# Kernel tuning notes

Measured on AMD Instinct MI355X. Metric: run time of the kernel, lower is better.

The kernel has to match this reference:

```python
import jax, jax.numpy as jnp
import numpy as np

N1 = 384
N2 = 384
E = 3072
NUM_LABELS = 32
GCN_SIZES = [128, 64, 32]
BIG = 99999.0


def gcn_conv(x, edge_index, w, b, n):
    # PyG GCNConv: add self-loops, symmetric deg^-1/2 normalization, x @ W then scatter-sum, + bias
    src, dst = edge_index[0], edge_index[1]
    loops = jnp.arange(n, dtype=src.dtype)
    src = jnp.concatenate([src, loops])
    dst = jnp.concatenate([dst, loops])
    deg = jax.ops.segment_sum(jnp.ones(src.shape[0], x.dtype), dst, num_segments=n)
    dinv = jnp.where(deg > 0, 1.0 / jnp.sqrt(deg), 0.0)
    norm = dinv[src] * dinv[dst]
    h = x @ w  # [n, out]
    return jax.ops.segment_sum(norm[:, None] * h[src], dst, num_segments=n) + b


def conv_pass(x, edge_index, ws, bs, n):
    feats = []
    for i in range(len(ws)):
        x = gcn_conv(x, edge_index, ws[i], bs[i], n)
        feats.append(x)
        if i < len(ws) - 1:
            x = jax.nn.relu(x)  # dropout inactive (eval mode)
    return feats


def build_cost_matrices(f1s, f2s, dels, inss, n1, n2):
    ins_const = BIG * (1.0 - jnp.eye(n1, dtype=jnp.float32))
    del_const = BIG * (1.0 - jnp.eye(n2, dtype=jnp.float32))
    mats = []
    for f1, f2, dp, ip in zip(f1s, f2s, dels, inss):
        main = -(f1 @ f2.T)                          # [n1, n2]
        del_sim = jnp.diag(-(f1 @ dp)) + ins_const   # [n1, n1]
        ins_sim = jnp.diag(-(f2 @ ip)) + del_const   # [n2, n2]
        dummy = jnp.zeros((n2, n1), jnp.float32)
        mats.append(jnp.block([[main, del_sim], [ins_sim, dummy]]))  # [n1+n2, n1+n2]
    return mats


def solve_lap(C):
    """Exact Jonker-Volgenant shortest-augmenting-path LAP (minimization),
    equivalent to lapjv / scipy linear_sum_assignment. Returns col4row."""
    C = np.asarray(C, dtype=np.float64)
    n = C.shape[0]
    u = np.zeros(n)
    v = np.zeros(n)
    row4col = np.full(n, -1, dtype=np.int64)
    col4row = np.full(n, -1, dtype=np.int64)
    for cur_row in range(n):
        shortest = np.full(n, np.inf)
        path = np.full(n, -1, dtype=np.int64)
        SR = np.zeros(n, dtype=bool)
        SC = np.zeros(n, dtype=bool)
        remaining = np.arange(n)
        num_rem = n
        min_val = 0.0
        i = cur_row
        sink = -1
        while sink == -1:
            SR[i] = True
            r = remaining[:num_rem]
            d = min_val + C[i, r] - u[i] - v[r]
            upd = d < shortest[r]
            ru = r[upd]
            shortest[ru] = d[upd]
            path[ru] = i
            k = int(np.argmin(shortest[r]))
            j = int(r[k])
            min_val = float(shortest[j])
            SC[j] = True
            num_rem -= 1
            remaining[k] = remaining[num_rem]
            if row4col[j] == -1:
                sink = j
            else:
                i = int(row4col[j])
        u[cur_row] += min_val
        other = SR.copy()
        other[cur_row] = False
        rows = np.nonzero(other)[0]
        if rows.size:
            u[rows] += min_val - shortest[col4row[rows]]
        cols = np.nonzero(SC)[0]
        v[cols] -= min_val - shortest[cols]
        j = sink
        while True:
            i = int(path[j])
            row4col[j] = i
            col4row[i], j = j, int(col4row[i])
            if i == cur_row:
                break
    return col4row


def setup_inputs() -> dict:
    key = jax.random.key(0)
    ks = jax.random.split(key, 24)
    inp = {}
    inp["edge_index_1"] = jax.random.randint(ks[0], (2, E), 0, N1, dtype=jnp.int32)
    inp["edge_index_2"] = jax.random.randint(ks[1], (2, E), 0, N2, dtype=jnp.int32)
    inp["features_1"] = jax.random.normal(ks[2], (N1, NUM_LABELS), jnp.float32)
    inp["features_2"] = jax.random.normal(ks[3], (N2, NUM_LABELS), jnp.float32)
    inp["n1"] = N1
    inp["n2"] = N2
    inp["avg_v"] = jnp.full((1,), (N1 + N2) / 2.0, jnp.float32)
    sizes = [NUM_LABELS] + GCN_SIZES
    for li in range(3):
        fan_in = sizes[li]
        inp[f"w{li+1}"] = jax.random.normal(ks[4 + 2 * li], (sizes[li], sizes[li + 1]), jnp.float32) / np.sqrt(fan_in)
        inp[f"b{li+1}"] = 0.01 * jax.random.normal(ks[5 + 2 * li], (sizes[li + 1],), jnp.float32)
        inp[f"del{li+1}"] = 0.1 * jax.random.normal(ks[10 + li], (GCN_SIZES[li],), jnp.float32)
        inp[f"ins{li+1}"] = 0.1 * jax.random.normal(ks[13 + li], (GCN_SIZES[li],), jnp.float32)
    inp["score_w"] = jax.random.normal(ks[16], (1, 3), jnp.float32) * 0.5
    inp["score_b"] = jax.random.normal(ks[17], (1,), jnp.float32) * 0.1
    return inp


def reference(edge_index_1, edge_index_2, features_1, features_2, n1, n2, avg_v,
              w1, b1, w2, b2, w3, b3, del1, del2, del3, ins1, ins2, ins3,
              score_w, score_b):
    ws, bs = (w1, w2, w3), (b1, b2, b3)
    f1s = conv_pass(features_1, edge_index_1, ws, bs, n1)
    f2s = conv_pass(features_2, edge_index_2, ws, bs, n2)
    mats = build_cost_matrices(f1s, f2s, (del1, del2, del3), (ins1, ins2, ins3), n1, n2)
    n = n1 + n2
    rows = jnp.arange(n)
    losses = []
    for S in mats:
        col = solve_lap(np.asarray(jax.device_get(S)))  # host LAP on detached costs
        losses.append(jnp.sum(S[rows, jnp.asarray(col, dtype=jnp.int32)]) / n)
    matching_cost = 2.0 * jnp.stack(losses) / (n1 + n2)  # [3]
    logits = score_w @ matching_cost + score_b           # [1]
    score = jax.nn.sigmoid(logits)
    pre_ged = -jnp.log(score) * avg_v                    # target_mode == 'exp'
    return score, pre_ged, matching_cost
```

## Files before the change

kernel.cpp:

```cpp
#include <hip/hip_runtime.h>
#include <math.h>


namespace {
constexpr int kN   = 384;
constexpr int kNN  = 768;
constexpr int kE   = 3072;
constexpr float kInf = 1e30f;
}

__device__ __forceinline__ float wave_min_bcast(float xv) {
    float v = xv;
    #define MSTAGE(ctrl) { int t = __builtin_amdgcn_update_dpp(__float_as_int(v), __float_as_int(v), ctrl, 0xF, 0xF, false); v = fminf(v, __int_as_float(t)); }
    MSTAGE(0x111); MSTAGE(0x112); MSTAGE(0x114); MSTAGE(0x118); MSTAGE(0x142); MSTAGE(0x143);
    #undef MSTAGE
    return __int_as_float(__builtin_amdgcn_readlane(__float_as_int(v), 63));
}

__device__ __forceinline__ float wave_sum_bcast(float x) {
    #define SSTAGE(ctrl) { int t = __builtin_amdgcn_update_dpp(0, __float_as_int(x), ctrl, 0xF, 0xF, false); x += __int_as_float(t); }
    SSTAGE(0x111); SSTAGE(0x112); SSTAGE(0x114); SSTAGE(0x118); SSTAGE(0x142); SSTAGE(0x143);
    #undef SSTAGE
    return __int_as_float(__builtin_amdgcn_readlane(__float_as_int(x), 63));
}

__device__ __forceinline__ void wave_min2_bcast(float m1, float m2, float& w1, float& w2) {
    const int INFB = __float_as_int(kInf);
    #define M2STAGE(ctrl) { \
        int t1 = __builtin_amdgcn_update_dpp(INFB, __float_as_int(m1), ctrl, 0xF, 0xF, false); \
        int t2 = __builtin_amdgcn_update_dpp(INFB, __float_as_int(m2), ctrl, 0xF, 0xF, false); \
        float o1 = __int_as_float(t1); float o2 = __int_as_float(t2); \
        float n2 = fminf(fmaxf(m1, o1), fminf(m2, o2)); \
        m1 = fminf(m1, o1); m2 = n2; }
    M2STAGE(0x111); M2STAGE(0x112); M2STAGE(0x114); M2STAGE(0x118); M2STAGE(0x142); M2STAGE(0x143);
    #undef M2STAGE
    w1 = __int_as_float(__builtin_amdgcn_readlane(__float_as_int(m1), 63));
    w2 = __int_as_float(__builtin_amdgcn_readlane(__float_as_int(m2), 63));
}


__global__ void init_deg(float* deg1, float* deg2) {
    int v = blockIdx.x * blockDim.x + threadIdx.x;
    if (v < kN) { deg1[v] = 1.0f; deg2[v] = 1.0f; }
}

__global__ void scatter_deg(const int* ei1, const int* ei2, float* deg1, float* deg2) {
    int e = blockIdx.x * blockDim.x + threadIdx.x;
    if (e < kE) {
        atomicAdd(&deg1[ei1[kE + e]], 1.0f);
    } else if (e < 2 * kE) {
        atomicAdd(&deg2[ei2[kE + (e - kE)]], 1.0f);
    }
}

__global__ void deg_to_dinv(float* deg1, float* deg2) {
    int v = blockIdx.x * blockDim.x + threadIdx.x;
    if (v < kN) { deg1[v] = rsqrtf(deg1[v]); deg2[v] = rsqrtf(deg2[v]); }
}


__global__ void gemm_act(const float* __restrict__ x, const float* __restrict__ w,
                         float* __restrict__ h, int FIN, int FOUT, int relu) {
    int idx = blockIdx.x * blockDim.x + threadIdx.x;
    if (idx >= kN * FOUT) return;
    int row = idx / FOUT;
    int oc  = idx - row * FOUT;
    float acc = 0.0f;
    for (int k = 0; k < FIN; ++k) {
        float xv = x[row * FIN + k];
        if (relu) xv = fmaxf(xv, 0.0f);
        acc += xv * w[k * FOUT + oc];
    }
    h[idx] = acc;
}

__global__ void agg_init(const float* __restrict__ h, const float* __restrict__ dinv,
                         const float* __restrict__ b, float* __restrict__ out, int F) {
    int idx = blockIdx.x * blockDim.x + threadIdx.x;
    if (idx >= kN * F) return;
    int v = idx / F;
    int f = idx - v * F;
    float dv = dinv[v];
    out[idx] = b[f] + dv * dv * h[idx];
}

__global__ void agg_edges(const int* __restrict__ ei, const float* __restrict__ h,
                          const float* __restrict__ dinv, float* __restrict__ out, int F) {
    int idx = blockIdx.x * blockDim.x + threadIdx.x;
    if (idx >= kE * F) return;
    int e = idx / F;
    int f = idx - e * F;
    int s = ei[e];
    int d = ei[kE + e];
    atomicAdd(&out[d * F + f], dinv[s] * dinv[d] * h[s * F + f]);
}


__global__ void node_dots(const float* __restrict__ f, const float* __restrict__ p,
                          float* __restrict__ out, int F) {
    int i = blockIdx.x * blockDim.x + threadIdx.x;
    if (i >= kN) return;
    float acc = 0.0f;
    for (int k = 0; k < F; ++k) acc += f[i * F + k] * p[k];
    out[i] = -acc;
}


__global__ void build_cost_red(const float* __restrict__ f1, const float* __restrict__ f2,
                               const float* __restrict__ D, const float* __restrict__ I,
                               float* __restrict__ C, float* __restrict__ CT, int have_ct,
                               unsigned* __restrict__ vbits, int F) {
    int j = blockIdx.x * blockDim.x + threadIdx.x;
    int i = blockIdx.y;
    if (j >= kN) return;
    float acc = 0.0f;
    for (int k = 0; k < F; ++k) acc += f1[i * F + k] * f2[j * F + k];
    float val = (-acc) - D[i] - I[j];
    float c = fminf(0.0f, val);
    C[i * kN + j] = c;
    if (have_ct) CT[(size_t)j * kN + i] = c;
    atomicMax(&vbits[j], __float_as_uint(c));
}


__global__ __launch_bounds__(64) void vb2v_scale(const unsigned* __restrict__ vbits,
                                                 float* __restrict__ v_sk,
                                                 float* __restrict__ s) {
    int m = blockIdx.x, lane = threadIdx.x;
    float a = 0.0f;
    for (int r = 0; r < 6; ++r) {
        int j = lane + 64 * r;
        float vv = __uint_as_float(vbits[m * kN + j]);
        v_sk[m * kN + j] = vv;
        a += fabsf(vv);
    }
    float tot = wave_sum_bcast(a);
    if (lane == 0) s[m] = fmaxf(tot / (float)kN, 1e-6f);
}

__global__ __launch_bounds__(64) void sk_row(const float* __restrict__ Call,
                                             const float* __restrict__ v_sk,
                                             float* __restrict__ u_sk,
                                             float tau, const float* __restrict__ s) {
    int i = blockIdx.x, m = blockIdx.y, lane = threadIdx.x;
    float t = tau * s[m];
    const float* R = Call + (size_t)m * kN * kN + (size_t)i * kN;
    float hh[6];
    float mn = kInf;
    #pragma unroll
    for (int r = 0; r < 6; ++r) {
        int j = lane + 64 * r;
        hh[r] = R[j] - v_sk[m * kN + j];
        mn = fminf(mn, hh[r]);
    }
    float wmn = wave_min_bcast(mn);
    float sm = 0.0f;
    #pragma unroll
    for (int r = 0; r < 6; ++r) sm += __expf((wmn - hh[r]) / t);
    float S = wave_sum_bcast(sm);
    if (lane == 0) u_sk[m * kN + i] = wmn - t * __logf(S);
}

__global__ __launch_bounds__(64) void sk_col(const float* __restrict__ Call,
                                             const float* __restrict__ CTall, int have_ct,
                                             const float* __restrict__ u_sk,
                                             float* __restrict__ v_sk,
                                             float tau, const float* __restrict__ s) {
    int j = blockIdx.x, m = blockIdx.y, lane = threadIdx.x;
    float t = tau * s[m];
    float hh[6];
    float mn = kInf;
    if (have_ct) {
        const float* R = CTall + (size_t)m * kN * kN + (size_t)j * kN;
        #pragma unroll
        for (int r = 0; r < 6; ++r) {
            int i = lane + 64 * r;
            hh[r] = R[i] - u_sk[m * kN + i];
            mn = fminf(mn, hh[r]);
        }
    } else {
        const float* Cm = Call + (size_t)m * kN * kN;
        #pragma unroll
        for (int r = 0; r < 6; ++r) {
            int i = lane + 64 * r;
            hh[r] = Cm[(size_t)i * kN + j] - u_sk[m * kN + i];
            mn = fminf(mn, hh[r]);
        }
    }
    float wmn = wave_min_bcast(mn);
    float sm = 0.0f;
    #pragma unroll
    for (int r = 0; r < 6; ++r) sm += __expf((wmn - hh[r]) / t);
    float S = wave_sum_bcast(sm);
    if (lane == 0) v_sk[m * kN + j] = wmn - t * __logf(S);
}

__global__ __launch_bounds__(64) void row_reduce(const float* __restrict__ Call,
                                                 const float* __restrict__ v_sk,
                                                 float* __restrict__ u0,
                                                 int* __restrict__ arg0) {
    int i = blockIdx.x, m = blockIdx.y, lane = threadIdx.x;
    const float* R = Call + (size_t)m * kN * kN + (size_t)i * kN;
    float m1 = kInf; int j1 = 0;
    #pragma unroll
    for (int r = 0; r < 6; ++r) {
        int j = lane + 64 * r;
        float h = R[j] - v_sk[m * kN + j];
        if (h < m1) { m1 = h; j1 = j; }
    }
    float w1 = wave_min_bcast(m1);
    unsigned long long mk = __ballot(m1 == w1);
    int jm = __builtin_amdgcn_readlane(j1, __ffsll(mk) - 1);
    if (lane == 0) { u0[m * kN + i] = w1; arg0[m * kN + i] = jm; }
}


__global__ __launch_bounds__(64) void lap384(const float* __restrict__ Call,
                                             const float* __restrict__ v_init,
                                             const float* __restrict__ u0,
                                             const int* __restrict__ arg0,
                                             const float* __restrict__ Dall,
                                             const float* __restrict__ Iall,
                                             float* __restrict__ loss_out) {
    const int m = blockIdx.x;
    const float* C = Call + (size_t)m * kN * kN;
    const int lane = threadIdx.x;

    __shared__ float u[kN], v[kN];
    __shared__ int xr[kN], yc[kN];
    __shared__ int2 sp[kN];
    __shared__ int2 steps[kN];
    __shared__ int2 yu[kN];
    __shared__ int2 rbatch[kN];
    __shared__ int flA[kN], flB[kN];
    __shared__ int fcl[kN];

    for (int j = lane; j < kN; j += 64) {
        v[j] = v_init[m * kN + j];
        xr[j] = -1; yc[j] = -1;
        yu[j] = make_int2(-1, 0);
        u[j] = u0[m * kN + j];
    }
    __syncthreads();

    float vreg[6];
    #pragma unroll
    for (int r = 0; r < 6; ++r) vreg[r] = v[lane + 64 * r];

    int nf = 0;
    #pragma unroll
    for (int r = 0; r < 6; ++r) {
        int i = lane + 64 * r;
        int j1 = arg0[m * kN + i];
        int old = atomicCAS(&yc[j1], -1, i);
        bool won = (old == -1);
        if (won) {
            xr[i] = j1;
            yu[j1] = make_int2(i, __float_as_int(u[i]));
        }
        unsigned long long mk = __ballot(!won);
        int pos = nf + (int)__popcll(mk & ((1ull << lane) - 1ull));
        if (!won) flA[pos] = i;
        nf += (int)__popcll(mk);
    }
    __syncthreads();

    int* src = flA; int* dst = flB;
    int f0 = nf;
    for (int pass = 0; pass < 2 && f0 > 0; ++pass) {
        int k = 0, f = 0, ops = 0;
        int i = -1;
        bool capped = false;
        for (;;) {
            if (i < 0) {
                if (k >= f0) break;
                i = src[k]; ++k;
            }
            if (++ops > 2 * kN) {
                if (lane == 0) dst[f] = i;
                ++f; capped = true; break;
            }
            const float* Crow = C + (size_t)i * kN;
            float m1 = kInf, m2 = kInf; int j1loc = 0;
            #pragma unroll
            for (int r = 0; r < 6; ++r) {
                int j = lane + 64 * r;
                float hh = Crow[j] - vreg[r];
                if (hh < m1) { m2 = m1; m1 = hh; j1loc = j; }
                else if (hh < m2) { m2 = hh; }
            }
            float w1, w2;
            wave_min2_bcast(m1, m2, w1, w2);
            unsigned long long mk = __ballot(m1 == w1);
            int j1 = __builtin_amdgcn_readlane(j1loc, __ffsll(mk) - 1);
            bool strict = (w1 < w2);
            int i0 = yc[j1];
            if (strict) {
                if (lane == (j1 & 63)) { vreg[j1 >> 6] -= (w2 - w1); v[j1] = vreg[j1 >> 6]; }
                if (lane == 0) {
                    xr[i] = j1; yc[j1] = i; u[i] = w2;
                    yu[j1] = make_int2(i, __float_as_int(w2));
                }
                i = (i0 >= 0) ? i0 : -1;
            } else {
                if (lane == 0) {
                    xr[i] = j1; yc[j1] = i; u[i] = w1;
                    yu[j1] = make_int2(i, __float_as_int(w1));
                }
                if (i0 >= 0) { if (lane == 0) dst[f] = i0; ++f; }
                i = -1;
            }
        }
        if (capped) {
            for (int t = k + lane; t < f0; t += 64) dst[f + (t - k)] = src[t];
            f += f0 - k;
        }
        int* tmp = src; src = dst; dst = tmp;
        f0 = f;
    }
    __syncthreads();

    {
        int fc = 0;
        for (int base = 0; base < kN; base += 64) {
            int j = base + lane;
            bool isfree = (yc[j] < 0);
            unsigned long long mk = __ballot(isfree);
            int pos = fc + __popcll(mk & ((1ull << lane) - 1ull));
            if (isfree) fcl[pos] = j;
            fc += (int)__popcll(mk);
        }
        __syncthreads();
        for (int t = lane; t < fc; t += 64) {
            int j = fcl[t];
            float mn = kInf;
            #pragma unroll 4
            for (int i = 0; i < kN; ++i)
                mn = fminf(mn, C[(size_t)i * kN + j] - u[i]);
            v[j] = mn;
        }
        __syncthreads();
    }

    const int nfree = f0;
    for (int fi = 0; fi < nfree; ++fi) {
        const int cur = src[fi];
        float sreg[6];
        unsigned scmask = 0;
        #pragma unroll
        for (int r = 0; r < 6; ++r) { sreg[r] = kInf; vreg[r] = v[lane + 64 * r]; }
        float min_val = 0.0f;
        int sink = -1;
        int scount = 0;
        int nbatch = 1;
        int iters = 0;
        int er = cur;
        int eu = __float_as_int(u[cur]);
        __syncthreads();

        while (true) {
            if (nbatch == 1) {
                float b0 = min_val - __int_as_float(eu);
                const float* R = C + (size_t)er * kN;
                float cc[6];
                #pragma unroll
                for (int r = 0; r < 6; ++r) cc[r] = R[lane + 64 * r];
                #pragma unroll
                for (int r = 0; r < 6; ++r) {
                    float d = b0 + cc[r] - vreg[r];
                    bool notsc = ((scmask >> r) & 1u) == 0u;
                    if (notsc && d < sreg[r]) {
                        sreg[r] = d;
                        sp[lane + 64 * r] = make_int2(__float_as_int(d), er);
                    }
                }
            } else {
                for (int t0 = 0; t0 < nbatch; t0 += 4) {
                    int2 e0 = rbatch[t0];
                    int2 e1 = rbatch[(t0 + 1 < nbatch) ? t0 + 1 : nbatch - 1];
                    int2 e2 = rbatch[(t0 + 2 < nbatch) ? t0 + 2 : nbatch - 1];
                    int2 e3 = rbatch[(t0 + 3 < nbatch) ? t0 + 3 : nbatch - 1];
                    float b0 = min_val - __int_as_float(e0.y);
                    float b1 = min_val - __int_as_float(e1.y);
                    float b2 = min_val - __int_as_float(e2.y);
                    float b3 = min_val - __int_as_float(e3.y);
                    const float* R0 = C + (size_t)e0.x * kN;
                    const float* R1 = C + (size_t)e1.x * kN;
                    const float* R2 = C + (size_t)e2.x * kN;
                    const float* R3 = C + (size_t)e3.x * kN;
                    float c0[6], c1[6], c2[6], c3[6];
                    #pragma unroll
                    for (int r = 0; r < 6; ++r) {
                        int j = lane + 64 * r;
                        c0[r] = R0[j]; c1[r] = R1[j]; c2[r] = R2[j]; c3[r] = R3[j];
                    }
                    #pragma unroll
                    for (int r = 0; r < 6; ++r) {
                        float db = sreg[r]; int pred = -1;
                        float d0 = b0 + c0[r] - vreg[r];
                        if (d0 < db) { db = d0; pred = e0.x; }
                        float d1 = b1 + c1[r] - vreg[r];
                        if (d1 < db) { db = d1; pred = e1.x; }
                        float d2 = b2 + c2[r] - vreg[r];
                        if (d2 < db) { db = d2; pred = e2.x; }
                        float d3 = b3 + c3[r] - vreg[r];
                        if (d3 < db) { db = d3; pred = e3.x; }
                        bool notsc = ((scmask >> r) & 1u) == 0u;
                        if (notsc && pred >= 0) {
                            sreg[r] = db;
                            sp[lane + 64 * r] = make_int2(__float_as_int(db), pred);
                        }
                    }
                }
            }

            float best = fminf(fminf(fminf(sreg[0], sreg[1]), fminf(sreg[2], sreg[3])),
                               fminf(sreg[4], sreg[5]));
            min_val = wave_min_bcast(best);
            if (!(min_val < kInf)) break;

            int myreg = -1, hits = 0;
            #pragma unroll
            for (int r = 0; r < 6; ++r) {
                if (sreg[r] == min_val) { if (myreg < 0) myreg = r; ++hits; }
            }
            unsigned long long hmk = __ballot(myreg >= 0);
            int nl = (int)__popcll(hmk);
            int L = __ffsll(hmk) - 1;
            int hcnt = __builtin_amdgcn_readlane(hits, L);
            if (nl == 1 && hcnt == 1) {
                int hreg = __builtin_amdgcn_readlane(myreg, L);
                int bj = L + 64 * hreg;
                if (lane == L) { sreg[hreg] = kInf; scmask |= 1u << hreg; }
                int2 p = yu[bj];
                if (lane == 0) steps[scount] = make_int2(p.x, bj);
                ++scount; nbatch = 1;
                er = p.x; eu = p.y;
                if (p.x < 0) sink = bj;
            } else {
                nbatch = 0;
                #pragma unroll
                for (int r = 0; r < 6; ++r) {
                    bool notsc = ((scmask >> r) & 1u) == 0u;
                    bool elig = notsc && (sreg[r] == min_val);
                    unsigned long long mk = __ballot(elig);
                    if (mk == 0) continue;
                    int j = lane + 64 * r;
                    int2 p = make_int2(0, 0);
                    if (elig) { p = yu[j]; sreg[r] = kInf; scmask |= 1u << r; }
                    int pos = (int)__popcll(mk & ((1ull << lane) - 1ull));
                    if (elig) {
                        steps[scount + pos] = make_int2(p.x, j);
                        rbatch[nbatch + pos] = p;
                    }
                    int cnt = (int)__popcll(mk);
                    unsigned long long fmk = __ballot(elig && p.x < 0);
                    if (fmk != 0 && sink < 0) sink = (__ffsll(fmk) - 1) + 64 * r;
                    scount += cnt; nbatch += cnt;
                }
            }
            if (sink >= 0) break;
            if (++iters > kN + 2) break;
            __syncthreads();
        }

        __syncthreads();
        if (sink >= 0) {
            for (int t = lane; t < scount; t += 64) {
                int2 sij = steps[t];
                int i = sij.x, jc = sij.y;
                float adj = min_val - __int_as_float(sp[jc].x);
                v[jc] -= adj;
                if (i >= 0) u[i] += adj;
            }
            if (lane == 0) u[cur] += min_val;
            __syncthreads();
            if (lane == 0) {
                int j = sink;
                int guard = 0;
                for (;;) {
                    int ii = sp[j].y;
                    yc[j] = ii;
                    int nxt = xr[ii];
                    xr[ii] = j;
                    j = nxt;
                    if (ii == cur) break;
                    if (++guard > kN) break;
                }
            }
            __syncthreads();
            for (int t = lane; t < scount; t += 64) {
                int jc = steps[t].y;
                int yy = yc[jc];
                yu[jc] = make_int2(yy, (yy >= 0) ? __float_as_int(u[yy]) : 0);
            }
            __syncthreads();
        }
    }

    float s = 0.0f;
    for (int t = lane; t < kN; t += 64) {
        int c_ = xr[t];
        if (c_ >= 0) s += C[(size_t)t * kN + c_];
        s += Dall[m * kN + t] + Iall[m * kN + t];
    }
    #pragma unroll
    for (int off = 32; off > 0; off >>= 1) s += __shfl_down(s, off);
    if (lane == 0) loss_out[m] = s;
}


__global__ void finalize(const float* __restrict__ loss_sums,
                         const float* __restrict__ score_w,
                         const float* __restrict__ score_b,
                         const float* __restrict__ avg_v,
                         float* __restrict__ out) {
    float mc[3];
    for (int m = 0; m < 3; ++m) mc[m] = 2.0f * (loss_sums[m] / (float)kNN) / (float)kNN;
    float logits = score_b[0];
    for (int m = 0; m < 3; ++m) logits += score_w[m] * mc[m];
    float score = 1.0f / (1.0f + expf(-logits));
    out[0] = score;
    out[1] = -logf(score) * avg_v[0];
    out[2] = mc[0];
    out[3] = mc[1];
    out[4] = mc[2];
}


extern "C" void kernel_launch(void* const* d_in, const int* in_sizes, int n_in,
                              void* d_out, int out_size, void* d_ws, size_t ws_size,
                              hipStream_t stream) {
    const int*   ei1 = (const int*)d_in[0];
    const int*   ei2 = (const int*)d_in[1];
    const float* x1  = (const float*)d_in[2];
    const float* x2  = (const float*)d_in[3];
    const float* avg = (const float*)d_in[6];

    const float *w[3], *b[3], *dl[3], *insp[3], *score_w, *score_b;
    if (in_sizes[11] == 8192) {
        w[0]=(const float*)d_in[7];  b[0]=(const float*)d_in[8];
        dl[0]=(const float*)d_in[9]; insp[0]=(const float*)d_in[10];
        w[1]=(const float*)d_in[11]; b[1]=(const float*)d_in[12];
        dl[1]=(const float*)d_in[13]; insp[1]=(const float*)d_in[14];
        w[2]=(const float*)d_in[15]; b[2]=(const float*)d_in[16];
        dl[2]=(const float*)d_in[17]; insp[2]=(const float*)d_in[18];
        score_w=(const float*)d_in[19]; score_b=(const float*)d_in[20];
    } else {
        w[0]=(const float*)d_in[7];  b[0]=(const float*)d_in[8];
        w[1]=(const float*)d_in[9];  b[1]=(const float*)d_in[10];
        w[2]=(const float*)d_in[11]; b[2]=(const float*)d_in[12];
        dl[0]=(const float*)d_in[13]; dl[1]=(const float*)d_in[14]; dl[2]=(const float*)d_in[15];
        insp[0]=(const float*)d_in[16]; insp[1]=(const float*)d_in[17]; insp[2]=(const float*)d_in[18];
        score_w=(const float*)d_in[19]; score_b=(const float*)d_in[20];
    }

    float* ws = (float*)d_ws;
    float* f1[3]  = { ws + 0,      ws + 49152,  ws + 73728  };
    float* f2[3]  = { ws + 86016,  ws + 135168, ws + 159744 };
    float* h      = ws + 172032;
    float* dinv1  = ws + 221184;
    float* dinv2  = ws + 221568;
    float* Dm     = ws + 221952;
    float* Im     = ws + 223104;
    unsigned* vbits = (unsigned*)(ws + 224256);
    float* C      = ws + 225408;
    float* loss   = ws + 667776;
    float* u_sk   = ws + 667792;
    float* v_sk   = ws + 668944;
    float* s_sk   = ws + 670096;
    float* u0     = ws + 670112;
    int*   arg0   = (int*)(ws + 671264);
    float* CT     = ws + 672416;
    const size_t need_ct = (672416 + 3 * (size_t)kN * kN) * sizeof(float);
    const int have_ct = (ws_size >= need_ct) ? 1 : 0;

    init_deg<<<6, 64, 0, stream>>>(dinv1, dinv2);
    scatter_deg<<<24, 256, 0, stream>>>(ei1, ei2, dinv1, dinv2);
    deg_to_dinv<<<6, 64, 0, stream>>>(dinv1, dinv2);

    const int Fs[3] = {128, 64, 32};
    for (int g = 0; g < 2; ++g) {
        const float* xin  = g ? x2  : x1;
        const int*   ei   = g ? ei2 : ei1;
        float*       dinv = g ? dinv2 : dinv1;
        float* const* f   = g ? f2 : f1;
        int fin = 32, relu = 0;
        for (int li = 0; li < 3; ++li) {
            int OF = Fs[li];
            int nthr = kN * OF;
            gemm_act<<<(nthr + 255) / 256, 256, 0, stream>>>(xin, w[li], h, fin, OF, relu);
            agg_init<<<(nthr + 255) / 256, 256, 0, stream>>>(h, dinv, b[li], f[li], OF);
            agg_edges<<<(kE * OF + 255) / 256, 256, 0, stream>>>(ei, h, dinv, f[li], OF);
            xin = f[li]; fin = OF; relu = 1;
        }
    }

    hipMemsetAsync(vbits, 0, 3 * kN * sizeof(unsigned), stream);

    for (int m = 0; m < 3; ++m) {
        node_dots<<<3, 128, 0, stream>>>(f1[m], dl[m],   Dm + m * kN, Fs[m]);
        node_dots<<<3, 128, 0, stream>>>(f2[m], insp[m], Im + m * kN, Fs[m]);
        build_cost_red<<<dim3(3, kN), 128, 0, stream>>>(f1[m], f2[m], Dm + m * kN,
                                                        Im + m * kN,
                                                        C + (size_t)m * kN * kN,
                                                        CT + (size_t)m * kN * kN, have_ct,
                                                        vbits + m * kN, Fs[m]);
    }

    vb2v_scale<<<3, 64, 0, stream>>>(vbits, v_sk, s_sk);
    float tau = 0.8f;
    for (int t = 0; t < 20; ++t) {
        sk_row<<<dim3(kN, 3), 64, 0, stream>>>(C, v_sk, u_sk, tau, s_sk);
        sk_col<<<dim3(kN, 3), 64, 0, stream>>>(C, CT, have_ct, u_sk, v_sk, tau, s_sk);
        tau *= 0.7f;
    }
    row_reduce<<<dim3(kN, 3), 64, 0, stream>>>(C, v_sk, u0, arg0);

    lap384<<<3, 64, 0, stream>>>(C, v_sk, u0, arg0, Dm, Im, loss);
    finalize<<<1, 1, 0, stream>>>(loss, score_w, score_b, avg, (float*)d_out);
}
```

Before: 2.449 ms.

## Batch GCN graphs and cost builds, fuse agg_init, retune Sinkhorn, defer free-column minima

Merges the GEMM and self-loop init into one kernel and runs both graphs in the same launch. Node dots and the three cost matrices are each built in a single batched launch. The Sinkhorn warm start drops from 20 to 16 iterations with faster tau decay. Inside the LAP kernel, free-column minimum recomputation moves into each augmentation and reads the transposed copy with float4 loads, and augmented columns are removed from the free list. This cuts launch count and uncoalesced strided reads, at the cost of repeated column scans per augmentation and a different warm-start quality.

```diff
diff --git a/kernel.cpp b/kernel.cpp
--- a/kernel.cpp
+++ b/kernel.cpp
@@ -59,8 +59,17 @@
 }
 
 
-__global__ void gemm_act(const float* __restrict__ x, const float* __restrict__ w,
-                         float* __restrict__ h, int FIN, int FOUT, int relu) {
+__global__ void gcn_layer(const float* __restrict__ x1in, const float* __restrict__ x2in,
+                          const float* __restrict__ w, const float* __restrict__ b,
+                          const float* __restrict__ dinv1, const float* __restrict__ dinv2,
+                          float* __restrict__ h1, float* __restrict__ h2,
+                          float* __restrict__ o1, float* __restrict__ o2,
+                          int FIN, int FOUT, int relu) {
+    int g = blockIdx.y;
+    const float* x    = g ? x2in : x1in;
+    const float* dinv = g ? dinv2 : dinv1;
+    float* h = g ? h2 : h1;
+    float* o = g ? o2 : o1;
     int idx = blockIdx.x * blockDim.x + threadIdx.x;
     if (idx >= kN * FOUT) return;
     int row = idx / FOUT;
@@ -72,20 +81,19 @@
         acc += xv * w[k * FOUT + oc];
     }
     h[idx] = acc;
-}
-
-__global__ void agg_init(const float* __restrict__ h, const float* __restrict__ dinv,
-                         const float* __restrict__ b, float* __restrict__ out, int F) {
-    int idx = blockIdx.x * blockDim.x + threadIdx.x;
-    if (idx >= kN * F) return;
-    int v = idx / F;
-    int f = idx - v * F;
-    float dv = dinv[v];
-    out[idx] = b[f] + dv * dv * h[idx];
-}
-
-__global__ void agg_edges(const int* __restrict__ ei, const float* __restrict__ h,
-                          const float* __restrict__ dinv, float* __restrict__ out, int F) {
+    float dv = dinv[row];
+    o[idx] = b[oc] + dv * dv * acc;
+}
+
+__global__ void agg_edges2(const int* __restrict__ ei1, const int* __restrict__ ei2,
+                           const float* __restrict__ h1, const float* __restrict__ h2,
+                           const float* __restrict__ dinv1, const float* __restrict__ dinv2,
+                           float* __restrict__ o1, float* __restrict__ o2, int F) {
+    int g = blockIdx.y;
+    const int* ei     = g ? ei2 : ei1;
+    const float* h    = g ? h2 : h1;
+    const float* dinv = g ? dinv2 : dinv1;
+    float* out = g ? o2 : o1;
     int idx = blockIdx.x * blockDim.x + threadIdx.x;
     if (idx >= kE * F) return;
     int e = idx / F;
@@ -96,30 +104,35 @@
 }
 
 
-__global__ void node_dots(const float* __restrict__ f, const float* __restrict__ p,
-                          float* __restrict__ out, int F) {
+struct DotJob { const float* f; const float* p; float* o; int F; };
+struct DotJobs { DotJob j[6]; };
+
+__global__ void node_dots_all(DotJobs jobs) {
+    DotJob jb = jobs.j[blockIdx.y];
     int i = blockIdx.x * blockDim.x + threadIdx.x;
     if (i >= kN) return;
     float acc = 0.0f;
-    for (int k = 0; k < F; ++k) acc += f[i * F + k] * p[k];
-    out[i] = -acc;
-}
-
-
-__global__ void build_cost_red(const float* __restrict__ f1, const float* __restrict__ f2,
-                               const float* __restrict__ D, const float* __restrict__ I,
-                               float* __restrict__ C, float* __restrict__ CT, int have_ct,
-                               unsigned* __restrict__ vbits, int F) {
+    for (int k = 0; k < jb.F; ++k) acc += jb.f[i * jb.F + k] * jb.p[k];
+    jb.o[i] = -acc;
+}
+
+
+struct CostJob { const float* f1; const float* f2; const float* D; const float* I;
+                 float* C; float* CT; unsigned* vb; int F; };
+struct CostJobs { CostJob j[3]; };
+
+__global__ void build_cost_all(CostJobs jobs, int have_ct) {
+    CostJob jb = jobs.j[blockIdx.z];
     int j = blockIdx.x * blockDim.x + threadIdx.x;
     int i = blockIdx.y;
     if (j >= kN) return;
     float acc = 0.0f;
-    for (int k = 0; k < F; ++k) acc += f1[i * F + k] * f2[j * F + k];
-    float val = (-acc) - D[i] - I[j];
+    for (int k = 0; k < jb.F; ++k) acc += jb.f1[i * jb.F + k] * jb.f2[j * jb.F + k];
+    float val = (-acc) - jb.D[i] - jb.I[j];
     float c = fminf(0.0f, val);
-    C[i * kN + j] = c;
-    if (have_ct) CT[(size_t)j * kN + i] = c;
-    atomicMax(&vbits[j], __float_as_uint(c));
+    jb.C[i * kN + j] = c;
+    if (have_ct) jb.CT[(size_t)j * kN + i] = c;
+    atomicMax(&jb.vb[j], __float_as_uint(c));
 }
 
 
@@ -216,6 +229,7 @@
 
 
 __global__ __launch_bounds__(64) void lap384(const float* __restrict__ Call,
+                                             const float* __restrict__ CTall, int have_ct,
                                              const float* __restrict__ v_init,
                                              const float* __restrict__ u0,
                                              const int* __restrict__ arg0,
@@ -223,7 +237,8 @@
                                              const float* __restrict__ Iall,
                                              float* __restrict__ loss_out) {
     const int m = blockIdx.x;
-    const float* C = Call + (size_t)m * kN * kN;
+    const float* C  = Call  + (size_t)m * kN * kN;
+    const float* CT = CTall + (size_t)m * kN * kN;
     const int lane = threadIdx.x;
 
     __shared__ float u[kN], v[kN];
@@ -234,6 +249,7 @@
     __shared__ int2 rbatch[kN];
     __shared__ int flA[kN], flB[kN];
     __shared__ int fcl[kN];
+    __shared__ int fc_sh;
 
     for (int j = lane; j < kN; j += 64) {
         v[j] = v_init[m * kN + j];
@@ -330,20 +346,37 @@
             if (isfree) fcl[pos] = j;
             fc += (int)__popcll(mk);
         }
-        __syncthreads();
-        for (int t = lane; t < fc; t += 64) {
-            int j = fcl[t];
-            float mn = kInf;
-            #pragma unroll 4
-            for (int i = 0; i < kN; ++i)
-                mn = fminf(mn, C[(size_t)i * kN + j] - u[i]);
-            v[j] = mn;
-        }
-        __syncthreads();
-    }
+        if (lane == 0) fc_sh = fc;
+    }
+    __syncthreads();
 
     const int nfree = f0;
     for (int fi = 0; fi < nfree; ++fi) {
+        {
+            int fc = fc_sh;
+            for (int t = lane; t < fc; t += 64) {
+                int j = fcl[t];
+                float mn = kInf;
+                if (have_ct) {
+                    const float4* Rt = (const float4*)(CT + (size_t)j * kN);
+                    #pragma unroll 4
+                    for (int q = 0; q < kN / 4; ++q) {
+                        float4 cv = Rt[q];
+                        mn = fminf(mn, cv.x - u[4 * q + 0]);
+                        mn = fminf(mn, cv.y - u[4 * q + 1]);
+                        mn = fminf(mn, cv.z - u[4 * q + 2]);
+                        mn = fminf(mn, cv.w - u[4 * q + 3]);
+                    }
+                } else {
+                    #pragma unroll 4
+                    for (int i = 0; i < kN; ++i)
+                        mn = fminf(mn, C[(size_t)i * kN + j] - u[i]);
+                }
+                v[j] = mn;
+            }
+        }
+        __syncthreads();
+
         const int cur = src[fi];
         float sreg[6];
         unsigned scmask = 0;
@@ -494,6 +527,16 @@
                 int yy = yc[jc];
                 yu[jc] = make_int2(yy, (yy >= 0) ? __float_as_int(u[yy]) : 0);
             }
+            {
+                int fcn = fc_sh;
+                int hit = -1;
+                for (int t = lane; t < fcn; t += 64) if (fcl[t] == sink) hit = t;
+                unsigned long long mk = __ballot(hit >= 0);
+                if (mk) {
+                    if (hit >= 0) fcl[hit] = fcl[fcn - 1];
+                    if (lane == __ffsll(mk) - 1) fc_sh = fcn - 1;
+                }
+            }
             __syncthreads();
         }
     }
@@ -558,21 +601,22 @@
     float* ws = (float*)d_ws;
     float* f1[3]  = { ws + 0,      ws + 49152,  ws + 73728  };
     float* f2[3]  = { ws + 86016,  ws + 135168, ws + 159744 };
-    float* h      = ws + 172032;
-    float* dinv1  = ws + 221184;
-    float* dinv2  = ws + 221568;
-    float* Dm     = ws + 221952;
-    float* Im     = ws + 223104;
-    unsigned* vbits = (unsigned*)(ws + 224256);
-    float* C      = ws + 225408;
-    float* loss   = ws + 667776;
-    float* u_sk   = ws + 667792;
-    float* v_sk   = ws + 668944;
-    float* s_sk   = ws + 670096;
-    float* u0     = ws + 670112;
-    int*   arg0   = (int*)(ws + 671264);
-    float* CT     = ws + 672416;
-    const size_t need_ct = (672416 + 3 * (size_t)kN * kN) * sizeof(float);
+    float* h1     = ws + 172032;
+    float* h2     = ws + 221184;
+    float* dinv1  = ws + 270336;
+    float* dinv2  = ws + 270720;
+    float* Dm     = ws + 271104;
+    float* Im     = ws + 272256;
+    unsigned* vbits = (unsigned*)(ws + 273408);
+    float* C      = ws + 274560;
+    float* loss   = ws + 716928;
+    float* u_sk   = ws + 716944;
+    float* v_sk   = ws + 718096;
+    float* s_sk   = ws + 719248;
+    float* u0     = ws + 719264;
+    int*   arg0   = (int*)(ws + 720416);
+    float* CT     = ws + 721568;
+    const size_t need_ct = (721568 + 3 * (size_t)kN * kN) * sizeof(float);
     const int have_ct = (ws_size >= need_ct) ? 1 : 0;
 
     init_deg<<<6, 64, 0, stream>>>(dinv1, dinv2);
@@ -580,43 +624,49 @@
     deg_to_dinv<<<6, 64, 0, stream>>>(dinv1, dinv2);
 
     const int Fs[3] = {128, 64, 32};
-    for (int g = 0; g < 2; ++g) {
-        const float* xin  = g ? x2  : x1;
-        const int*   ei   = g ? ei2 : ei1;
-        float*       dinv = g ? dinv2 : dinv1;
-        float* const* f   = g ? f2 : f1;
+    {
+        const float* xin1 = x1;
+        const float* xin2 = x2;
         int fin = 32, relu = 0;
         for (int li = 0; li < 3; ++li) {
             int OF = Fs[li];
             int nthr = kN * OF;
-            gemm_act<<<(nthr + 255) / 256, 256, 0, stream>>>(xin, w[li], h, fin, OF, relu);
-            agg_init<<<(nthr + 255) / 256, 256, 0, stream>>>(h, dinv, b[li], f[li], OF);
-            agg_edges<<<(kE * OF + 255) / 256, 256, 0, stream>>>(ei, h, dinv, f[li], OF);
-            xin = f[li]; fin = OF; relu = 1;
+            gcn_layer<<<dim3((nthr + 255) / 256, 2), 256, 0, stream>>>(
+                xin1, xin2, w[li], b[li], dinv1, dinv2, h1, h2, f1[li], f2[li], fin, OF, relu);
+            agg_edges2<<<dim3((kE * OF + 255) / 256, 2), 256, 0, stream>>>(
+                ei1, ei2, h1, h2, dinv1, dinv2, f1[li], f2[li], OF);
+            xin1 = f1[li]; xin2 = f2[li]; fin = OF; relu = 1;
         }
     }
 
     hipMemsetAsync(vbits, 0, 3 * kN * sizeof(unsigned), stream);
 
-    for (int m = 0; m < 3; ++m) {
-        node_dots<<<3, 128, 0, stream>>>(f1[m], dl[m],   Dm + m * kN, Fs[m]);
-        node_dots<<<3, 128, 0, stream>>>(f2[m], insp[m], Im + m * kN, Fs[m]);
-        build_cost_red<<<dim3(3, kN), 128, 0, stream>>>(f1[m], f2[m], Dm + m * kN,
-                                                        Im + m * kN,
-                                                        C + (size_t)m * kN * kN,
-                                                        CT + (size_t)m * kN * kN, have_ct,
-                                                        vbits + m * kN, Fs[m]);
+    {
+        DotJobs dj;
+        for (int m = 0; m < 3; ++m) {
+            dj.j[m]     = { f1[m], dl[m],   Dm + m * kN, Fs[m] };
+            dj.j[3 + m] = { f2[m], insp[m], Im + m * kN, Fs[m] };
+        }
+        node_dots_all<<<dim3(3, 6), 128, 0, stream>>>(dj);
+
+        CostJobs cj;
+        for (int m = 0; m < 3; ++m) {
+            cj.j[m] = { f1[m], f2[m], Dm + m * kN, Im + m * kN,
+                        C + (size_t)m * kN * kN, CT + (size_t)m * kN * kN,
+                        vbits + m * kN, Fs[m] };
+        }
+        build_cost_all<<<dim3(3, kN, 3), 128, 0, stream>>>(cj, have_ct);
     }
 
     vb2v_scale<<<3, 64, 0, stream>>>(vbits, v_sk, s_sk);
     float tau = 0.8f;
-    for (int t = 0; t < 20; ++t) {
+    for (int t = 0; t < 16; ++t) {
         sk_row<<<dim3(kN, 3), 64, 0, stream>>>(C, v_sk, u_sk, tau, s_sk);
         sk_col<<<dim3(kN, 3), 64, 0, stream>>>(C, CT, have_ct, u_sk, v_sk, tau, s_sk);
-        tau *= 0.7f;
+        tau *= 0.62f;
     }
     row_reduce<<<dim3(kN, 3), 64, 0, stream>>>(C, v_sk, u0, arg0);
 
-    lap384<<<3, 64, 0, stream>>>(C, v_sk, u0, arg0, Dm, Im, loss);
+    lap384<<<3, 64, 0, stream>>>(C, CT, have_ct, v_sk, u0, arg0, Dm, Im, loss);
     finalize<<<1, 1, 0, stream>>>(loss, score_w, score_b, avg, (float*)d_out);
 }
```

New measurement: 2.331 ms. 1.05x faster.
